# Optimization experiments

Measured on AMD Instinct MI355X. Metric: run time of the kernel, lower is better.

The kernel has to match this reference:

```python
import jax, jax.numpy as jnp
import numpy as np

NSAMPLE = 32  # knn neighbors (init kwarg nsample)
BN_EPS = 1e-5


def _mlp_layer(x, w, b, g, beta, m, v):
    # x: [B,S,K,Cin]; 1x1 conv == channel matmul, then eval-mode BN, then ReLU
    h = jnp.einsum('bskc,oc->bsko', x, w) + b
    h = (h - m) * (g * jax.lax.rsqrt(v + BN_EPS)) + beta
    return jax.nn.relu(h)


def setup_inputs() -> dict:
    key = jax.random.key(0)
    ks = jax.random.split(key, 8)
    B, N, D, S = 8, 16384, 64, 2048
    inp = {
        'xyz': jax.random.normal(ks[0], (B, N, 3), jnp.float32),
        'points': jax.random.normal(ks[1], (B, N, D), jnp.float32),
        'sample_idx': jax.random.randint(ks[2], (S,), 0, N, jnp.int32),
        'w0': jax.random.normal(ks[3], (64, 64), jnp.float32) * 0.1,
        'b0': jnp.zeros((64,), jnp.float32),
        'g0': jnp.ones((64,), jnp.float32),
        'beta0': jnp.zeros((64,), jnp.float32),
        'm0': jnp.zeros((64,), jnp.float32),
        'v0': jnp.ones((64,), jnp.float32),
        'w1': jax.random.normal(ks[4], (64, 64), jnp.float32) * 0.1,
        'b1': jnp.zeros((64,), jnp.float32),
        'g1': jnp.ones((64,), jnp.float32),
        'beta1': jnp.zeros((64,), jnp.float32),
        'm1': jnp.zeros((64,), jnp.float32),
        'v1': jnp.ones((64,), jnp.float32),
        'w2': jax.random.normal(ks[5], (128, 64), jnp.float32) * 0.1,
        'b2': jnp.zeros((128,), jnp.float32),
        'g2': jnp.ones((128,), jnp.float32),
        'beta2': jnp.zeros((128,), jnp.float32),
        'm2': jnp.zeros((128,), jnp.float32),
        'v2': jnp.ones((128,), jnp.float32),
    }
    return inp


def reference(xyz, points, sample_idx,
              w0, b0, g0, beta0, m0, v0,
              w1, b1, g1, beta1, m1, v1,
              w2, b2, g2, beta2, m2, v2):
    # subsample (torch.randperm analogue, shared across batch)
    new_xyz = xyz[:, sample_idx, :]            # [B,S,3]
    new_pts = points[:, sample_idx, :]         # [B,S,D]
    # squared distances in feature space: [B,S,N]
    d = (jnp.sum(new_pts * new_pts, -1)[:, :, None]
         - 2.0 * jnp.einsum('bsd,bnd->bsn', new_pts, points)
         + jnp.sum(points * points, -1)[:, None, :])
    _, idx = jax.lax.top_k(-d, NSAMPLE)        # k smallest -> [B,S,K]
    # gather neighbors: [B,S,K,D]
    grouped = jax.vmap(lambda p, i: p[i])(points, idx)
    h = _mlp_layer(grouped, w0, b0, g0, beta0, m0, v0)
    h = _mlp_layer(h, w1, b1, g1, beta1, m1, v1)
    h = _mlp_layer(h, w2, b2, g2, beta2, m2, v2)
    new_points = jnp.max(h, axis=2)            # max over neighbors -> [B,S,128]
    return (new_xyz, new_points)
```

## Files before the change

### kernel.cpp

```cpp
#include <hip/hip_runtime.h>

#define B_  8
#define N_  16384
#define D_  64
#define S_  2048
#define K_  32
#define SPLIT_  4
#define NSPL_   (N_/SPLIT_)
#define CH32_   (NSPL_/32)
#define PLANE_  ((size_t)B_*N_*64)

using short8_ = __attribute__((ext_vector_type(8))) short;
using f32x4_  = __attribute__((ext_vector_type(4))) float;

__device__ __forceinline__ void bf3split(float f, short& h0, short& h1, short& h2)
{
  unsigned u0 = __float_as_uint(f);
  float f0 = __uint_as_float(u0 & 0xFFFF0000u);
  h0 = (short)(u0 >> 16);
  float r1 = f - f0;
  unsigned u1 = __float_as_uint(r1);
  float f1 = __uint_as_float(u1 & 0xFFFF0000u);
  h1 = (short)(u1 >> 16);
  float r2 = r1 - f1;
  h2 = (short)(__float_as_uint(r2) >> 16);
}

__device__ __forceinline__ void bf2split8(const float* f, short8_& h0, short8_& h1)
{
  #pragma unroll
  for (int j = 0; j < 8; ++j) {
    unsigned u = __float_as_uint(f[j]);
    h0[j] = (short)(u >> 16);
    float r = f[j] - __uint_as_float(u & 0xFFFF0000u);
    h1[j] = (short)(__float_as_uint(r) >> 16);
  }
}

__device__ __forceinline__ void insert32(float (&Lv)[32], int (&Li)[32], float x, int n)
{
  bool ci = x < Lv[0];
  #pragma unroll
  for (int i = 0; i < 31; ++i) {
    bool c1 = x < Lv[i+1];
    float nv = c1 ? Lv[i+1] : (ci ? x : Lv[i]);
    int   ni = c1 ? Li[i+1] : (ci ? n : Li[i]);
    Lv[i] = nv; Li[i] = ni;
    ci = c1;
  }
  Lv[31] = ci ? x : Lv[31];
  Li[31] = ci ? n : Li[31];
}

__global__ __launch_bounds__(256) void k_prep(
    const float* __restrict__ xyz, const float* __restrict__ points,
    const int* __restrict__ sidx, float* __restrict__ out, float* __restrict__ sqn,
    short* __restrict__ P0, short* __restrict__ P1, short* __restrict__ P2)
{
  int tid = blockIdx.x * 256 + threadIdx.x;
  const float4* p = (const float4*)(points + (size_t)tid * 64);

  float s = 0.f;
  #pragma unroll
  for (int i = 0; i < 16; ++i) {
    float4 v = p[i];
    s += v.x*v.x + v.y*v.y + v.z*v.z + v.w*v.w;
  }
  sqn[tid] = s;

  int n = tid & (N_-1);
  int c = n >> 6, ct = (n >> 4) & 3, mc = n & 15;
  size_t segbase = (((size_t)(tid >> 14) * 256 + c) * 4 + ct) * 2;

  #pragma unroll
  for (int g = 0; g < 8; ++g) {
    float4 a = p[2*g], b4 = p[2*g+1];
    float f[8] = {a.x,a.y,a.z,a.w, b4.x,b4.y,b4.z,b4.w};
    short8_ h0v, h1v, h2v;
    #pragma unroll
    for (int j = 0; j < 8; ++j) {
      short h0, h1, h2;
      bf3split(f[j], h0, h1, h2);
      h0v[j] = h0; h1v[j] = h1; h2v[j] = h2;
    }
    size_t off = ((segbase + (g>>2))*64 + (size_t)(g&3)*16 + mc)*8;
    *(short8_*)(P0 + off) = h0v;
    *(short8_*)(P1 + off) = h1v;
    *(short8_*)(P2 + off) = h2v;
  }
  if (tid < B_*S_) {
    int b = tid >> 11, ss = tid & (S_-1);
    int nn = sidx[ss];
    const float* src = xyz + ((size_t)b * N_ + nn) * 3;
    out[(size_t)tid*3+0] = src[0];
    out[(size_t)tid*3+1] = src[1];
    out[(size_t)tid*3+2] = src[2];
  }
}

__global__ __launch_bounds__(256) void k_knn(
    const short* __restrict__ P0, const short* __restrict__ P1,
    const short* __restrict__ P2, const int* __restrict__ sidx,
    const float* __restrict__ sqn, uint2* __restrict__ pw)
{
  __shared__ __align__(16) char smraw[33280];
  float* Dtr = (float*)smraw;
  uint2* qb  = (uint2*)(smraw + 9216);

  const int t = threadIdx.x;
  const int b     = blockIdx.x & 7;
  const int y     = blockIdx.x >> 3;
  const int tile  = y & 31;
  const int split = y >> 5;
  const int s0 = tile * 64;
  const float* Qb = sqn + (size_t)b * N_;

  const int lane = t & 63, wv = t >> 6;
  const int quad = lane >> 4, mcol = lane & 15;

  short8_ A0[2], A1[2], A2[2];
  {
    int srow = sidx[s0 + 16*wv + mcol];
    int cs = srow >> 6, cts = (srow >> 4) & 3, ms = srow & 15;
    size_t ab = (((size_t)(b*256 + cs))*4 + cts)*2*512 + ((size_t)quad*16 + ms)*8;
    #pragma unroll
    for (int kt = 0; kt < 2; ++kt) {
      A0[kt] = *(const short8_*)(P0 + ab + kt*512);
      A1[kt] = *(const short8_*)(P1 + ab + kt*512);
      A2[kt] = *(const short8_*)(P2 + ab + kt*512);
    }
  }

  float Lv[32]; int Li[32];
  #pragma unroll
  for (int i = 0; i < 32; ++i) { Lv[i] = 3.0e38f; Li[i] = 0; }

  const int r = t >> 2;
  const int q = t & 3;
  const int n0base = split * NSPL_;
  const size_t bc8base = (size_t)b * 256;

  int qhead = 0, qtail = 0;

  auto do_select = [&](int n0sel) {
    if (__any((qtail - qhead) >= 2)) {
      if (qhead < qtail) {
        uint2 e = qb[(qhead & 7)*256 + t];
        qhead++;
        float x = __uint_as_float(e.x);
        if (x < Lv[0])
          insert32(Lv, Li, x, (int)e.y);
      }
    }
    float ownL0 = Lv[0];
    float tmin = ownL0;
    tmin = fminf(tmin, __shfl_xor(tmin, 1));
    tmin = fminf(tmin, __shfl_xor(tmin, 2));
    float t24 = Lv[24];
    t24 = fmaxf(t24, __shfl_xor(t24, 1));
    t24 = fmaxf(t24, __shfl_xor(t24, 2));
    const float thr = fminf(fminf(tmin, t24), ownL0);

    float4 ka = *(const float4*)(Dtr + r*36 + q*8);
    float4 kb = *(const float4*)(Dtr + r*36 + q*8 + 4);
    float x8[8] = {ka.x,ka.y,ka.z,ka.w, kb.x,kb.y,kb.z,kb.w};
    unsigned m = 0;
    #pragma unroll
    for (int i = 0; i < 8; ++i)
      m |= (x8[i] < thr) ? (1u << i) : 0u;
    while (m) {
      int i = __ffs(m) - 1;
      m &= m - 1;
      float xlo = (i & 1) ? ((i & 2) ? x8[3] : x8[1]) : ((i & 2) ? x8[2] : x8[0]);
      float xhi = (i & 1) ? ((i & 2) ? x8[7] : x8[5]) : ((i & 2) ? x8[6] : x8[4]);
      float x = (i & 4) ? xhi : xlo;
      if (qtail - qhead >= 8) {
        uint2 e = qb[(qhead & 7)*256 + t];
        qhead++;
        float xe = __uint_as_float(e.x);
        if (xe < Lv[0])
          insert32(Lv, Li, xe, (int)e.y);
      }
      qb[(qtail & 7)*256 + t] = make_uint2(__float_as_uint(x), (unsigned)(n0sel + q*8 + i));
      qtail++;
    }
  };

  size_t goff = ((bc8base + (size_t)(n0base >> 6)) * 8) * 512 + (size_t)lane * 8;

  for (int ch = 0; ch < CH32_; ++ch) {
    const int n0 = n0base + ch * 32;

    short8_ b0[2][2], b1[2][2], b2[2][2];
    #pragma unroll
    for (int s = 0; s < 4; ++s) {
      b0[s>>1][s&1] = *(const short8_*)(P0 + goff + (size_t)s*512);
      b1[s>>1][s&1] = *(const short8_*)(P1 + goff + (size_t)s*512);
      b2[s>>1][s&1] = *(const short8_*)(P2 + goff + (size_t)s*512);
    }
    float sq0 = Qb[n0 + mcol];
    float sq1 = Qb[n0 + 16 + mcol];
    goff += 2048;

    if (ch > 0) do_select(n0 - 32);

    #pragma unroll
    for (int ct = 0; ct < 2; ++ct) {
      f32x4_ a = {0.f, 0.f, 0.f, 0.f};
      #pragma unroll
      for (int kt = 0; kt < 2; ++kt) {
        a = __builtin_amdgcn_mfma_f32_16x16x32_bf16(A0[kt], b0[ct][kt], a, 0,0,0);
        a = __builtin_amdgcn_mfma_f32_16x16x32_bf16(A0[kt], b1[ct][kt], a, 0,0,0);
        a = __builtin_amdgcn_mfma_f32_16x16x32_bf16(A1[kt], b0[ct][kt], a, 0,0,0);
        a = __builtin_amdgcn_mfma_f32_16x16x32_bf16(A1[kt], b1[ct][kt], a, 0,0,0);
        a = __builtin_amdgcn_mfma_f32_16x16x32_bf16(A0[kt], b2[ct][kt], a, 0,0,0);
        a = __builtin_amdgcn_mfma_f32_16x16x32_bf16(A2[kt], b0[ct][kt], a, 0,0,0);
        a = __builtin_amdgcn_mfma_f32_16x16x32_bf16(A1[kt], b2[ct][kt], a, 0,0,0);
        a = __builtin_amdgcn_mfma_f32_16x16x32_bf16(A2[kt], b1[ct][kt], a, 0,0,0);
      }
      int cc = 16*ct + mcol;
      float sq = ct ? sq1 : sq0;
      int rb = 16*wv + 4*quad;
      Dtr[(rb+0)*36 + cc] = sq - 2.f*a[0];
      Dtr[(rb+1)*36 + cc] = sq - 2.f*a[1];
      Dtr[(rb+2)*36 + cc] = sq - 2.f*a[2];
      Dtr[(rb+3)*36 + cc] = sq - 2.f*a[3];
    }
  }
  do_select(n0base + NSPL_ - 32);

  while (__any(qhead < qtail)) {
    if (qhead < qtail) {
      uint2 e = qb[(qhead & 7)*256 + t];
      qhead++;
      float x = __uint_as_float(e.x);
      if (x < Lv[0])
        insert32(Lv, Li, x, (int)e.y);
    }
  }

  uint2* mbuf = (uint2*)smraw;
  const int rowg = b * S_ + s0;
  for (int pass = 0; pass < 2; ++pass) {
    __syncthreads();
    const int rb = pass * 32;
    if (r >= rb && r < rb + 32) {
      #pragma unroll
      for (int i = 0; i < 32; ++i)
        mbuf[(r - rb)*130 + q*32 + (31 - i)] =
            make_uint2(__float_as_uint(Lv[i]), (unsigned)Li[i]);
    }
    __syncthreads();
    if (t < 32) {
      const uint2* Lrow = mbuf + t*130;
      uint2* dst = pw + ((size_t)(rowg + rb + t) * SPLIT_ + split) * 32;
      int p0 = 0, p1 = 0, p2 = 0, p3 = 0;
      for (int k = 0; k < 32; ++k) {
        float bv = 3.0e38f; unsigned bi = 0xFFFFFFFFu; int bq = 0;
        int pa[4] = {p0, p1, p2, p3};
        #pragma unroll
        for (int q4 = 0; q4 < 4; ++q4) {
          if (pa[q4] < 32) {
            uint2 e = Lrow[q4*32 + pa[q4]];
            float v = __uint_as_float(e.x);
            if (v < bv || (v == bv && e.y < bi)) { bv = v; bi = e.y; bq = q4; }
          }
        }
        dst[k] = make_uint2(__float_as_uint(bv), bi);
        if (bq == 0) p0++; else if (bq == 1) p1++; else if (bq == 2) p2++; else p3++;
      }
    }
  }
}

__global__ __launch_bounds__(256) void k_prep_fb(
    const float* __restrict__ xyz, const float* __restrict__ points,
    const int* __restrict__ sidx, float* __restrict__ out, float* __restrict__ sqn)
{
  int tid = blockIdx.x * 256 + threadIdx.x;
  const float4* p = (const float4*)(points + (size_t)tid * 64);
  float s = 0.f;
  #pragma unroll
  for (int i = 0; i < 16; ++i) {
    float4 v = p[i];
    s += v.x*v.x + v.y*v.y + v.z*v.z + v.w*v.w;
  }
  sqn[tid] = s;
  if (tid < B_*S_) {
    int b = tid >> 11, ss = tid & (S_-1);
    int n = sidx[ss];
    const float* src = xyz + ((size_t)b * N_ + n) * 3;
    out[(size_t)tid*3+0] = src[0];
    out[(size_t)tid*3+1] = src[1];
    out[(size_t)tid*3+2] = src[2];
  }
}

__global__ __launch_bounds__(256) void k_knn_fb(
    const float* __restrict__ points, const int* __restrict__ sidx,
    const float* __restrict__ sqn, uint2* __restrict__ pw)
{
  __shared__ __align__(16) char smraw[45312];
  short* Bp0 = (short*)smraw;
  short* Bp1 = (short*)(smraw + 9216);
  short* Bp2 = (short*)(smraw + 18432);
  float* Dt  = (float*)(smraw + 27648);
  float* sqc = (float*)(smraw + 45056);

  const int t = threadIdx.x;
  const int b     = blockIdx.x & 7;
  const int y     = blockIdx.x >> 3;
  const int tile  = y & 31;
  const int split = y >> 5;
  const int s0 = tile * 64;
  const float* Pb = points + (size_t)b * N_ * 64;
  const float* Qb = sqn    + (size_t)b * N_;

  const int lane = t & 63, wv = t >> 6;
  const int quad = lane >> 4, mcol = lane & 15;

  short8_ A0[2], A1[2], A2[2];
  {
    int srow = sidx[s0 + 16*wv + mcol];
    const float* ar = Pb + (size_t)srow * 64;
    #pragma unroll
    for (int kt = 0; kt < 2; ++kt) {
      float4 v0 = *(const float4*)(ar + 32*kt + 8*quad);
      float4 v1 = *(const float4*)(ar + 32*kt + 8*quad + 4);
      float f[8] = {v0.x,v0.y,v0.z,v0.w,v1.x,v1.y,v1.z,v1.w};
      #pragma unroll
      for (int j = 0; j < 8; ++j) {
        short h0, h1, h2;
        bf3split(f[j], h0, h1, h2);
        A0[kt][j] = h0; A1[kt][j] = h1; A2[kt][j] = h2;
      }
    }
  }

  float Lv[32]; int Li[32];
  #pragma unroll
  for (int i = 0; i < 32; ++i) { Lv[i] = 3.0e38f; Li[i] = 0; }

  const int r = t >> 2;
  const int q = t & 3;
  const int n0base = split * NSPL_;

  for (int ch = 0; ch < NSPL_/64; ++ch) {
    const int n0 = n0base + ch * 64;
    {
      const int n = t & 63, jg = t >> 6;
      const float* src = Pb + (size_t)(n0 + n) * 64 + 16*jg;
      float4 u0 = *(const float4*)(src);
      float4 u1 = *(const float4*)(src + 4);
      float4 u2 = *(const float4*)(src + 8);
      float4 u3 = *(const float4*)(src + 12);
      float f[16] = {u0.x,u0.y,u0.z,u0.w, u1.x,u1.y,u1.z,u1.w,
                     u2.x,u2.y,u2.z,u2.w, u3.x,u3.y,u3.z,u3.w};
      short8_ p0[2], p1[2], p2[2];
      #pragma unroll
      for (int j = 0; j < 16; ++j) {
        short h0, h1, h2;
        bf3split(f[j], h0, h1, h2);
        p0[j>>3][j&7] = h0; p1[j>>3][j&7] = h1; p2[j>>3][j&7] = h2;
      }
      *(short8_*)(Bp0 + n*72 + 16*jg)     = p0[0];
      *(short8_*)(Bp0 + n*72 + 16*jg + 8) = p0[1];
      *(short8_*)(Bp1 + n*72 + 16*jg)     = p1[0];
      *(short8_*)(Bp1 + n*72 + 16*jg + 8) = p1[1];
      *(short8_*)(Bp2 + n*72 + 16*jg)     = p2[0];
      *(short8_*)(Bp2 + n*72 + 16*jg + 8) = p2[1];
      if (t < 16) *(float4*)(sqc + 4*t) = *(const float4*)(Qb + n0 + 4*t);
    }
    __syncthreads();

    f32x4_ acc[4];
    #pragma unroll
    for (int ct = 0; ct < 4; ++ct) {
      const int boff = (16*ct + mcol)*72 + 8*quad;
      short8_ b0[2], b1[2], b2[2];
      b0[0] = *(const short8_*)(Bp0 + boff); b0[1] = *(const short8_*)(Bp0 + boff + 32);
      b1[0] = *(const short8_*)(Bp1 + boff); b1[1] = *(const short8_*)(Bp1 + boff + 32);
      b2[0] = *(const short8_*)(Bp2 + boff); b2[1] = *(const short8_*)(Bp2 + boff + 32);
      f32x4_ a = {0.f, 0.f, 0.f, 0.f};
      #pragma unroll
      for (int kt = 0; kt < 2; ++kt) {
        a = __builtin_amdgcn_mfma_f32_16x16x32_bf16(A0[kt], b0[kt], a, 0,0,0);
        a = __builtin_amdgcn_mfma_f32_16x16x32_bf16(A0[kt], b1[kt], a, 0,0,0);
        a = __builtin_amdgcn_mfma_f32_16x16x32_bf16(A1[kt], b0[kt], a, 0,0,0);
        a = __builtin_amdgcn_mfma_f32_16x16x32_bf16(A1[kt], b1[kt], a, 0,0,0);
        a = __builtin_amdgcn_mfma_f32_16x16x32_bf16(A0[kt], b2[kt], a, 0,0,0);
        a = __builtin_amdgcn_mfma_f32_16x16x32_bf16(A2[kt], b0[kt], a, 0,0,0);
        a = __builtin_amdgcn_mfma_f32_16x16x32_bf16(A1[kt], b2[kt], a, 0,0,0);
        a = __builtin_amdgcn_mfma_f32_16x16x32_bf16(A2[kt], b1[kt], a, 0,0,0);
      }
      acc[ct] = a;
    }
    #pragma unroll
    for (int ct = 0; ct < 4; ++ct) {
      int c = 16*ct + mcol;
      float sq = sqc[c];
      float4 kv;
      kv.x = sq - 2.f*acc[ct][0];
      kv.y = sq - 2.f*acc[ct][1];
      kv.z = sq - 2.f*acc[ct][2];
      kv.w = sq - 2.f*acc[ct][3];
      *(float4*)(Dt + c*68 + 16*wv + 4*quad) = kv;
    }
    __syncthreads();

    float L0 = Lv[0];
    L0 = fminf(L0, __shfl_xor(L0, 1));
    L0 = fminf(L0, __shfl_xor(L0, 2));
    const float tau = L0;
    #pragma unroll
    for (int g = 0; g < 4; ++g) {
      #pragma unroll
      for (int u = 0; u < 4; ++u) {
        int c = q*16 + g*4 + u;
        float x = Dt[c*68 + r];
        if (x < fminf(tau, Lv[0]))
          insert32(Lv, Li, x, n0 + c);
      }
    }
  }

  uint2* mbuf = (uint2*)smraw;
  const int rowg = b * S_ + s0;
  for (int pass = 0; pass < 2; ++pass) {
    __syncthreads();
    const int rb = pass * 32;
    if (r >= rb && r < rb + 32) {
      #pragma unroll
      for (int i = 0; i < 32; ++i)
        mbuf[(r - rb)*130 + q*32 + (31 - i)] =
            make_uint2(__float_as_uint(Lv[i]), (unsigned)Li[i]);
    }
    __syncthreads();
    if (t < 32) {
      const uint2* Lrow = mbuf + t*130;
      uint2* dst = pw + ((size_t)(rowg + rb + t) * SPLIT_ + split) * 32;
      int p0 = 0, p1 = 0, p2 = 0, p3 = 0;
      for (int k = 0; k < 32; ++k) {
        float bv = 3.0e38f; unsigned bi = 0xFFFFFFFFu; int bq = 0;
        int pa[4] = {p0, p1, p2, p3};
        #pragma unroll
        for (int q4 = 0; q4 < 4; ++q4) {
          if (pa[q4] < 32) {
            uint2 e = Lrow[q4*32 + pa[q4]];
            float v = __uint_as_float(e.x);
            if (v < bv || (v == bv && e.y < bi)) { bv = v; bi = e.y; bq = q4; }
          }
        }
        dst[k] = make_uint2(__float_as_uint(bv), bi);
        if (bq == 0) p0++; else if (bq == 1) p1++; else if (bq == 2) p2++; else p3++;
      }
    }
  }
}

__global__ __launch_bounds__(256) void k_sel(const uint2* __restrict__ pw,
                                             int* __restrict__ nbr)
{
  int row = blockIdx.x * 256 + threadIdx.x;
  const uint2* L = pw + (size_t)row * (SPLIT_*32);
  int* dst = nbr + (size_t)row * K_;
  int p[4] = {0,0,0,0};
  for (int k = 0; k < K_; ++k) {
    float bv = 3.0e38f; unsigned bi = 0xFFFFFFFFu; int bq = 0;
    #pragma unroll
    for (int q4 = 0; q4 < 4; ++q4) {
      if (p[q4] < 32) {
        uint2 e = L[q4*32 + p[q4]];
        float v = __uint_as_float(e.x);
        if (v < bv || (v == bv && e.y < bi)) { bv = v; bi = e.y; bq = q4; }
      }
    }
    dst[k] = (int)bi;
    p[bq]++;
  }
}

__device__ __forceinline__ void layer_mfma(
    int lane, int wv, const float* Xf, float* Hf,
    const float* __restrict__ wgt, const float* scl, const float* bia)
{
  const int quad = lane >> 4, mcol = lane & 15;
  const int o = wv*16 + mcol;
  const float sc = scl[o];
  short8_ B0[2], B1[2];
  #pragma unroll
  for (int kt = 0; kt < 2; ++kt) {
    const float* wp = wgt + o*64 + kt*32 + quad*8;
    float4 u0 = *(const float4*)(wp);
    float4 u1 = *(const float4*)(wp + 4);
    float f[8] = {u0.x*sc,u0.y*sc,u0.z*sc,u0.w*sc,
                  u1.x*sc,u1.y*sc,u1.z*sc,u1.w*sc};
    bf2split8(f, B0[kt], B1[kt]);
  }
  const float bo = bia[o];
  const int kt2 = (o >> 5) & 1, qk2 = (o >> 3) & 3, h2 = (o >> 2) & 1, j2 = o & 3;
  #pragma unroll
  for (int mt = 0; mt < 2; ++mt) {
    short8_ A0[2], A1[2];
    #pragma unroll
    for (int kt = 0; kt < 2; ++kt) {
      float4 x0 = *(const float4*)(Xf + (((mt*2+kt)*2+0)*256) + lane*4);
      float4 x1 = *(const float4*)(Xf + (((mt*2+kt)*2+1)*256) + lane*4);
      float f[8] = {x0.x,x0.y,x0.z,x0.w, x1.x,x1.y,x1.z,x1.w};
      bf2split8(f, A0[kt], A1[kt]);
    }
    f32x4_ a = {0.f, 0.f, 0.f, 0.f};
    #pragma unroll
    for (int kt = 0; kt < 2; ++kt) {
      a = __builtin_amdgcn_mfma_f32_16x16x32_bf16(A0[kt], B0[kt], a, 0,0,0);
      a = __builtin_amdgcn_mfma_f32_16x16x32_bf16(A0[kt], B1[kt], a, 0,0,0);
      a = __builtin_amdgcn_mfma_f32_16x16x32_bf16(A1[kt], B0[kt], a, 0,0,0);
    }
    #pragma unroll
    for (int reg = 0; reg < 4; ++reg) {
      int ml = quad*4 + reg;
      float hval = fmaxf(a[reg] + bo, 0.f);
      Hf[((mt*2 + kt2)*2 + h2)*256 + (qk2*16 + ml)*4 + j2] = hval;
    }
  }
}

__global__ __launch_bounds__(256) void k_mlp(
    const float* __restrict__ points, const int* __restrict__ nbr,
    const float* __restrict__ w0, const float* __restrict__ b0,
    const float* __restrict__ g0, const float* __restrict__ be0,
    const float* __restrict__ m0, const float* __restrict__ v0,
    const float* __restrict__ w1, const float* __restrict__ b1,
    const float* __restrict__ g1, const float* __restrict__ be1,
    const float* __restrict__ m1, const float* __restrict__ v1,
    const float* __restrict__ w2, const float* __restrict__ b2,
    const float* __restrict__ g2, const float* __restrict__ be2,
    const float* __restrict__ m2, const float* __restrict__ v2,
    float* __restrict__ out)
{
  __shared__ __align__(16) float Xf[2048];
  __shared__ __align__(16) float Hf[2048];
  __shared__ float scl[128];
  __shared__ float bia[128];
  __shared__ int   nIx[32];

  const int t  = threadIdx.x;
  const int bs = blockIdx.x;
  const int b  = bs >> 11;
  const int lane = t & 63, wv = t >> 6;
  const int quad = lane >> 4, mcol = lane & 15;

  if (t < 32) nIx[t] = nbr[(size_t)bs * K_ + t];
  if (t >= 64 && t < 128) {
    int i = t - 64;
    float sc = g0[i] * rsqrtf(v0[i] + 1e-5f);
    scl[i] = sc;
    bia[i] = (b0[i] - m0[i]) * sc + be0[i];
  }
  __syncthreads();
  #pragma unroll
  for (int rep = 0; rep < 2; ++rep) {
    int task = rep*256 + t;
    int row = task >> 4, j4 = task & 15;
    float4 v = *(const float4*)(points + ((size_t)b*N_ + nIx[row])*64 + j4*4);
    int kt = j4 >> 3, qk = (j4 >> 1) & 3, h = j4 & 1;
    *(float4*)(Xf + (((row>>4)*2 + kt)*2 + h)*256 + (qk*16 + (row&15))*4) = v;
  }
  __syncthreads();

  layer_mfma(lane, wv, Xf, Hf, w0, scl, bia);
  __syncthreads();
  if (t < 64) {
    float sc = g1[t] * rsqrtf(v1[t] + 1e-5f);
    scl[t] = sc;
    bia[t] = (b1[t] - m1[t]) * sc + be1[t];
  }
  __syncthreads();
  layer_mfma(lane, wv, Hf, Xf, w1, scl, bia);
  __syncthreads();
  if (t < 128) {
    float sc = g2[t] * rsqrtf(v2[t] + 1e-5f);
    scl[t] = sc;
    bia[t] = (b2[t] - m2[t]) * sc + be2[t];
  }
  __syncthreads();

  short8_ A0[2][2], A1[2][2];
  #pragma unroll
  for (int mt = 0; mt < 2; ++mt)
    #pragma unroll
    for (int kt = 0; kt < 2; ++kt) {
      float4 x0 = *(const float4*)(Xf + (((mt*2+kt)*2+0)*256) + lane*4);
      float4 x1 = *(const float4*)(Xf + (((mt*2+kt)*2+1)*256) + lane*4);
      float f[8] = {x0.x,x0.y,x0.z,x0.w, x1.x,x1.y,x1.z,x1.w};
      bf2split8(f, A0[mt][kt], A1[mt][kt]);
    }
  float* outp = out + (size_t)(B_*S_)*3 + (size_t)bs*128;
  #pragma unroll
  for (int sub = 0; sub < 2; ++sub) {
    const int o = (wv*2 + sub)*16 + mcol;
    const float sc = scl[o];
    short8_ B0[2], B1[2];
    #pragma unroll
    for (int kt = 0; kt < 2; ++kt) {
      const float* wp = w2 + o*64 + kt*32 + quad*8;
      float4 u0 = *(const float4*)(wp);
      float4 u1 = *(const float4*)(wp + 4);
      float f[8] = {u0.x*sc,u0.y*sc,u0.z*sc,u0.w*sc,
                    u1.x*sc,u1.y*sc,u1.z*sc,u1.w*sc};
      bf2split8(f, B0[kt], B1[kt]);
    }
    float vmax = -3.0e38f;
    #pragma unroll
    for (int mt = 0; mt < 2; ++mt) {
      f32x4_ a = {0.f, 0.f, 0.f, 0.f};
      #pragma unroll
      for (int kt = 0; kt < 2; ++kt) {
        a = __builtin_amdgcn_mfma_f32_16x16x32_bf16(A0[mt][kt], B0[kt], a, 0,0,0);
        a = __builtin_amdgcn_mfma_f32_16x16x32_bf16(A0[mt][kt], B1[kt], a, 0,0,0);
        a = __builtin_amdgcn_mfma_f32_16x16x32_bf16(A1[mt][kt], B0[kt], a, 0,0,0);
      }
      vmax = fmaxf(vmax, fmaxf(fmaxf(a[0], a[1]), fmaxf(a[2], a[3])));
    }
    vmax = fmaxf(vmax, __shfl_xor(vmax, 16));
    vmax = fmaxf(vmax, __shfl_xor(vmax, 32));
    if (quad == 0) outp[o] = fmaxf(vmax + bia[o], 0.f);
  }
}

extern "C" void kernel_launch(void* const* d_in, const int* in_sizes, int n_in,
                              void* d_out, int out_size, void* d_ws, size_t ws_size,
                              hipStream_t stream)
{
  const float* xyz  = (const float*)d_in[0];
  const float* pts  = (const float*)d_in[1];
  const int*   sidx = (const int*)  d_in[2];
  const float* w0 = (const float*)d_in[3];
  const float* b0 = (const float*)d_in[4];
  const float* g0 = (const float*)d_in[5];
  const float* be0= (const float*)d_in[6];
  const float* m0 = (const float*)d_in[7];
  const float* v0 = (const float*)d_in[8];
  const float* w1 = (const float*)d_in[9];
  const float* b1 = (const float*)d_in[10];
  const float* g1 = (const float*)d_in[11];
  const float* be1= (const float*)d_in[12];
  const float* m1 = (const float*)d_in[13];
  const float* v1 = (const float*)d_in[14];
  const float* w2 = (const float*)d_in[15];
  const float* b2 = (const float*)d_in[16];
  const float* g2 = (const float*)d_in[17];
  const float* be2= (const float*)d_in[18];
  const float* m2 = (const float*)d_in[19];
  const float* v2 = (const float*)d_in[20];

  float* out = (float*)d_out;
  float* sqn = (float*)d_ws;
  int*   nbr = (int*)  ((char*)d_ws + (size_t)B_*N_*4);
  uint2* pw  = (uint2*)((char*)d_ws + (size_t)B_*N_*4 + (size_t)B_*S_*K_*4);
  char*  pl  = (char*)d_ws + (size_t)B_*N_*4 + (size_t)B_*S_*K_*4
             + (size_t)B_*S_*SPLIT_*32*8;
  short* P0 = (short*)pl;
  short* P1 = P0 + PLANE_;
  short* P2 = P1 + PLANE_;
  const size_t need = (size_t)B_*N_*4 + (size_t)B_*S_*K_*4
                    + (size_t)B_*S_*SPLIT_*32*8 + 3*PLANE_*2;

  if (ws_size >= need) {
    k_prep<<<(B_*N_)/256, 256, 0, stream>>>(xyz, pts, sidx, out, sqn, P0, P1, P2);
    k_knn <<<B_*32*SPLIT_, 256, 0, stream>>>(P0, P1, P2, sidx, sqn, pw);
  } else {
    k_prep_fb<<<(B_*N_)/256, 256, 0, stream>>>(xyz, pts, sidx, out, sqn);
    k_knn_fb <<<B_*32*SPLIT_, 256, 0, stream>>>(pts, sidx, sqn, pw);
  }
  k_sel <<<(B_*S_)/256, 256, 0, stream>>>(pw, nbr);
  k_mlp <<<B_*S_, 256, 0, stream>>>(pts, nbr,
            w0,b0,g0,be0,m0,v0, w1,b1,g1,be1,m1,v1, w2,b2,g2,be2,m2,v2, out);
}
```

Before: 827.1 us.

## Restructure KNN candidate queue drain, cache threshold, and raise MFMA priority

The candidate-selection step now counts the passing candidates with a popcount and drains the per-thread queue up front in a wavefront-uniform loop, then enqueues them with a branchless unrolled loop instead of the data-dependent ffs loop. The cross-lane threshold (min of L0 and max of L24 across the 4 threads) is recomputed only on every other chunk and cached in between. Global loads switch to byte-offset base pointers with int offsets. The MFMA block is wrapped in s_setprio to favour the matrix work. The stale threshold may let more candidates through, and the uniform drain can make lanes wait on each other.

```diff
diff --git a/kernel.cpp b/kernel.cpp
--- a/kernel.cpp
+++ b/kernel.cpp
@@ -113,7 +113,6 @@
   const int tile  = y & 31;
   const int split = y >> 5;
   const int s0 = tile * 64;
-  const float* Qb = sqn + (size_t)b * N_;
 
   const int lane = t & 63, wv = t >> 6;
   const int quad = lane >> 4, mcol = lane & 15;
@@ -141,8 +140,17 @@
   const size_t bc8base = (size_t)b * 256;
 
   int qhead = 0, qtail = 0;
-
-  auto do_select = [&](int n0sel) {
+  float thr = 3.0e38f;
+
+  const size_t blkbase = ((bc8base + (size_t)(n0base >> 6)) * 8) * 512 * 2;
+  const char* P0c = (const char*)P0 + blkbase;
+  const char* P1c = (const char*)P1 + blkbase;
+  const char* P2c = (const char*)P2 + blkbase;
+  const char* Qc  = (const char*)(sqn + (size_t)b * N_ + n0base);
+  const int lo16 = lane * 16;
+  const int mo4  = mcol * 4;
+
+  auto do_select = [&](int n0sel, bool refresh) {
     if (__any((qtail - qhead) >= 2)) {
       if (qhead < qtail) {
         uint2 e = qb[(qhead & 7)*256 + t];
@@ -152,14 +160,16 @@
           insert32(Lv, Li, x, (int)e.y);
       }
     }
-    float ownL0 = Lv[0];
-    float tmin = ownL0;
-    tmin = fminf(tmin, __shfl_xor(tmin, 1));
-    tmin = fminf(tmin, __shfl_xor(tmin, 2));
-    float t24 = Lv[24];
-    t24 = fmaxf(t24, __shfl_xor(t24, 1));
-    t24 = fmaxf(t24, __shfl_xor(t24, 2));
-    const float thr = fminf(fminf(tmin, t24), ownL0);
+    if (refresh) {
+      float tmin = Lv[0];
+      tmin = fminf(tmin, __shfl_xor(tmin, 1));
+      tmin = fminf(tmin, __shfl_xor(tmin, 2));
+      float t24 = Lv[24];
+      t24 = fmaxf(t24, __shfl_xor(t24, 1));
+      t24 = fmaxf(t24, __shfl_xor(t24, 2));
+      thr = fminf(tmin, t24);
+    }
+    const float th = fminf(thr, Lv[0]);
 
     float4 ka = *(const float4*)(Dtr + r*36 + q*8);
     float4 kb = *(const float4*)(Dtr + r*36 + q*8 + 4);
@@ -167,43 +177,46 @@
     unsigned m = 0;
     #pragma unroll
     for (int i = 0; i < 8; ++i)
-      m |= (x8[i] < thr) ? (1u << i) : 0u;
-    while (m) {
-      int i = __ffs(m) - 1;
-      m &= m - 1;
-      float xlo = (i & 1) ? ((i & 2) ? x8[3] : x8[1]) : ((i & 2) ? x8[2] : x8[0]);
-      float xhi = (i & 1) ? ((i & 2) ? x8[7] : x8[5]) : ((i & 2) ? x8[6] : x8[4]);
-      float x = (i & 4) ? xhi : xlo;
-      if (qtail - qhead >= 8) {
+      m |= (x8[i] < th) ? (1u << i) : 0u;
+
+    int cnt = __popc(m);
+    while (__any(qtail - qhead + cnt > 8)) {
+      if (qtail - qhead + cnt > 8) {
         uint2 e = qb[(qhead & 7)*256 + t];
         qhead++;
         float xe = __uint_as_float(e.x);
         if (xe < Lv[0])
           insert32(Lv, Li, xe, (int)e.y);
       }
-      qb[(qtail & 7)*256 + t] = make_uint2(__float_as_uint(x), (unsigned)(n0sel + q*8 + i));
-      qtail++;
+    }
+    #pragma unroll
+    for (int i = 0; i < 8; ++i) {
+      if (m & (1u << i)) {
+        qb[(qtail & 7)*256 + t] =
+            make_uint2(__float_as_uint(x8[i]), (unsigned)(n0sel + q*8 + i));
+        qtail++;
+      }
     }
   };
-
-  size_t goff = ((bc8base + (size_t)(n0base >> 6)) * 8) * 512 + (size_t)lane * 8;
 
   for (int ch = 0; ch < CH32_; ++ch) {
     const int n0 = n0base + ch * 32;
+    const int cb = ch*4096 + lo16;
 
     short8_ b0[2][2], b1[2][2], b2[2][2];
     #pragma unroll
     for (int s = 0; s < 4; ++s) {
-      b0[s>>1][s&1] = *(const short8_*)(P0 + goff + (size_t)s*512);
-      b1[s>>1][s&1] = *(const short8_*)(P1 + goff + (size_t)s*512);
-      b2[s>>1][s&1] = *(const short8_*)(P2 + goff + (size_t)s*512);
-    }
-    float sq0 = Qb[n0 + mcol];
-    float sq1 = Qb[n0 + 16 + mcol];
-    goff += 2048;
-
-    if (ch > 0) do_select(n0 - 32);
-
+      b0[s>>1][s&1] = *(const short8_*)(P0c + cb + s*1024);
+      b1[s>>1][s&1] = *(const short8_*)(P1c + cb + s*1024);
+      b2[s>>1][s&1] = *(const short8_*)(P2c + cb + s*1024);
+    }
+    const int qo = ch*128 + mo4;
+    float sq0 = *(const float*)(Qc + qo);
+    float sq1 = *(const float*)(Qc + qo + 64);
+
+    if (ch > 0) do_select(n0 - 32, (ch & 1) != 0);
+
+    __builtin_amdgcn_s_setprio(1);
     #pragma unroll
     for (int ct = 0; ct < 2; ++ct) {
       f32x4_ a = {0.f, 0.f, 0.f, 0.f};
@@ -226,8 +239,9 @@
       Dtr[(rb+2)*36 + cc] = sq - 2.f*a[2];
       Dtr[(rb+3)*36 + cc] = sq - 2.f*a[3];
     }
-  }
-  do_select(n0base + NSPL_ - 32);
+    __builtin_amdgcn_s_setprio(0);
+  }
+  do_select(n0base + NSPL_ - 32, true);
 
   while (__any(qhead < qtail)) {
     if (qhead < qtail) {
```

Result: slower. 930.1 us (+12.5%).
